# Optimization experiments

Measured on AMD Instinct MI355X. Metric: run time of the kernel, lower is better.

The kernel has to match this reference:

```python
import jax, jax.numpy as jnp
import numpy as np

N_HEAD = 16
WINDOW = 16  # fixed_window_size


def setup_inputs() -> dict:
    key = jax.random.key(0)
    k1, k2, k3 = jax.random.split(key, 3)
    B, T, C = 2, 2048, 1024
    x = jax.random.normal(k1, (B, T, C), dtype=jnp.float32)
    # torch Linear(C, 3C, bias=False): y = x @ W.T with W [3C, C].
    # We store the pre-transposed [C, 3C] matrix so y = x @ w_qkv.
    w_qkv = jax.random.normal(k2, (C, 3 * C), dtype=jnp.float32) * (1.0 / np.sqrt(C))
    w_proj = jax.random.normal(k3, (C, C), dtype=jnp.float32) * (1.0 / np.sqrt(C))
    return {"x": x, "w_qkv": w_qkv, "w_proj": w_proj}


def reference(x, w_qkv, w_proj):
    B, T, C = x.shape
    H, D = N_HEAD, C // N_HEAD
    qkv = x @ w_qkv  # [B, T, 3C]
    q, k, v = jnp.split(qkv, 3, axis=-1)
    # [B, T, C] -> [B, H, T, D]
    q, k, v = (t.reshape(B, T, H, D).transpose(0, 2, 1, 3) for t in (q, k, v))
    att = jnp.einsum("bhtd,bhsd->bhts", q, k) * (1.0 / np.sqrt(D))  # [B,H,T,T]
    # Mask exactly as the torch module builds it: tril ones, then zero where
    # col - row >= fixed_window_size (note: col-row, per the source).
    row = jnp.arange(T)[:, None]
    col = jnp.arange(T)[None, :]
    mask = (col <= row) & ~(col - row >= WINDOW)  # [T, T] bool
    att = jnp.where(mask[None, None, :, :], att, -jnp.inf)
    att = jax.nn.softmax(att, axis=-1)
    y = jnp.einsum("bhts,bhsd->bhtd", att, v)  # [B,H,T,D]
    y = y.transpose(0, 2, 1, 3).reshape(B, T, C)
    return y @ w_proj
```

## Files before the change

### kernel.cpp

```cpp
#include <hip/hip_runtime.h>
#include <stdint.h>

#define LOG2E 1.4426950408889634f
#define QSCALE 0.18033688011112042f

typedef __attribute__((ext_vector_type(8))) short bf16x8;
typedef __attribute__((ext_vector_type(4))) float f32x4;
typedef __attribute__((ext_vector_type(8))) unsigned short u16x8;

#define B_ 2
#define T_ 2048
#define C_ 1024
#define H_ 16
#define D_ 64
#define BT_ 4096
#define N3_ 3072

#if __has_builtin(__builtin_amdgcn_exp2f)
#define EXP2(x) __builtin_amdgcn_exp2f(x)
#else
#define EXP2(x) exp2f(x)
#endif

__device__ __forceinline__ unsigned short f2bf(float f) {
  union { float f; unsigned u; } x; x.f = f;
  return (unsigned short)((x.u + 0x7fffu + ((x.u >> 16) & 1u)) >> 16);
}
__device__ __forceinline__ float bf2f(unsigned short u) {
  union { unsigned u; float f; } x; x.u = ((unsigned)u) << 16;
  return x.f;
}
__device__ __forceinline__ unsigned f2u(float f) {
  union { float f; unsigned u; } x; x.f = f; return x.u;
}
__device__ __forceinline__ unsigned pack_bf2(float a, float b) {
  return __builtin_amdgcn_perm(f2u(b) + 0x8000u, f2u(a) + 0x8000u, 0x07060302u);
}

__device__ __forceinline__ void gld16(const unsigned short* g, unsigned short* l) {
  __builtin_amdgcn_global_load_lds(
      (const __attribute__((address_space(1))) unsigned int*)g,
      (__attribute__((address_space(3))) unsigned int*)l, 16, 0, 0);
}

__device__ __forceinline__ void tr32(const float* __restrict__ in,
                                     unsigned short* __restrict__ out,
                                     int K, int N, int b, int nbx, int tid) {
  __shared__ unsigned short tile[32][33];
  const int bx = b % nbx, by = b / nbx;
  const int n0 = bx * 32, k0 = by * 32;
  const int tx = tid & 31, ty = (tid >> 5) * 4;
#pragma unroll
  for (int r = 0; r < 4; r++)
    tile[ty + r][tx] = f2bf(in[(size_t)(k0 + ty + r) * N + n0 + tx]);
  __syncthreads();
#pragma unroll
  for (int r = 0; r < 4; r++)
    out[(size_t)(n0 + ty + r) * K + k0 + tx] = tile[tx][ty + r];
}

__global__ __launch_bounds__(256) void prep_kernel(
    const float* __restrict__ x, unsigned short* __restrict__ xb,
    const float* __restrict__ wq, unsigned short* __restrict__ wqT,
    const float* __restrict__ wp, unsigned short* __restrict__ wpT) {
  const int bid = blockIdx.x, tid = threadIdx.x;
  if (bid < 4096) {
    int i = (bid * 256 + tid) * 4;
    float4 v = *(const float4*)(x + i);
    ushort4 o;
    o.x = f2bf(v.x); o.y = f2bf(v.y); o.z = f2bf(v.z); o.w = f2bf(v.w);
    *(ushort4*)(xb + i) = o;
  } else if (bid < 4096 + 3072) {
    tr32(wq, wqT, 1024, 3072, bid - 4096, 96, tid);
  } else {
    tr32(wp, wpT, 1024, 1024, bid - 7168, 32, tid);
  }
}

template <int MODE>
__global__ __launch_bounds__(256) void gemm_kernel(
    const unsigned short* __restrict__ A, const unsigned short* __restrict__ Bt,
    unsigned short* __restrict__ qo, unsigned short* __restrict__ ko,
    unsigned short* __restrict__ vo, float* __restrict__ fo) {
  __shared__ unsigned short As[128 * 64];
  const int tid = threadIdx.x;
  const int wave = tid >> 6, lane = tid & 63;
  const int quad = lane >> 4, l16 = lane & 15;
  const int wm = (wave >> 1) * 64, wn = (wave & 1) * 32;
  const int m0 = blockIdx.y * 128, n0 = blockIdx.x * 64;

  f32x4 acc[4][2] = {};

  const unsigned short* Bp0 = Bt + (size_t)(n0 + wn + l16) * 1024 + quad * 8;
  const unsigned short* Bp1 = Bp0 + 16 * 1024;

  for (int k = 0; k < 1024; k += 64) {
    __syncthreads();
#pragma unroll
    for (int i = 0; i < 4; i++) {
      const int s = tid + 256 * i;
      const int row = s >> 3, ch = s & 7;
      gld16(A + (size_t)(m0 + row) * 1024 + k + ((ch ^ (row & 7)) * 8), As + s * 8);
    }
    bf16x8 b00 = *(const bf16x8*)(Bp0 + k);
    bf16x8 b01 = *(const bf16x8*)(Bp1 + k);
    bf16x8 b10 = *(const bf16x8*)(Bp0 + k + 32);
    bf16x8 b11 = *(const bf16x8*)(Bp1 + k + 32);
    __syncthreads();
#pragma unroll
    for (int sub = 0; sub < 2; sub++) {
      bf16x8 af[4];
#pragma unroll
      for (int mi = 0; mi < 4; mi++) {
        const int row = wm + mi * 16 + l16;
        af[mi] = *(const bf16x8*)(As + row * 64 + (((sub * 4 + quad) ^ (row & 7)) * 8));
      }
      const bf16x8 bz0 = sub ? b10 : b00;
      const bf16x8 bz1 = sub ? b11 : b01;
#pragma unroll
      for (int mi = 0; mi < 4; mi++) {
        acc[mi][0] = __builtin_amdgcn_mfma_f32_16x16x32_bf16(af[mi], bz0, acc[mi][0], 0, 0, 0);
        acc[mi][1] = __builtin_amdgcn_mfma_f32_16x16x32_bf16(af[mi], bz1, acc[mi][1], 0, 0, 0);
      }
    }
  }

  if (MODE == 0) {
    const int part = n0 >> 10;
    const int hh = (n0 >> 6) & 15;
#pragma unroll
    for (int mi = 0; mi < 4; mi++) {
#pragma unroll
      for (int r = 0; r < 4; r++) {
        const int m = m0 + wm + mi * 16 + quad * 4 + r;
        const int b = m >> 11, t = m & 2047;
#pragma unroll
        for (int ni = 0; ni < 2; ni++) {
          const int d = wn + ni * 16 + l16;
          float val = acc[mi][ni][r];
          if (part == 0) val *= QSCALE;
          const unsigned short bv = f2bf(val);
          if (part == 0)
            qo[((size_t)(b * H_ + hh) * T_ + t) * D_ + d] = bv;
          else if (part == 1)
            ko[((size_t)(b * H_ + hh) * T_ + t) * D_ + d] = bv;
          else
            vo[((size_t)(b * H_ + hh) * D_ + d) * T_ + t] = bv;
        }
      }
    }
  } else {
#pragma unroll
    for (int mi = 0; mi < 4; mi++)
#pragma unroll
      for (int r = 0; r < 4; r++) {
        const int m = m0 + wm + mi * 16 + quad * 4 + r;
#pragma unroll
        for (int ni = 0; ni < 2; ni++)
          fo[(size_t)m * 1024 + n0 + wn + ni * 16 + l16] = acc[mi][ni][r];
      }
  }
}

__global__ __launch_bounds__(256) void attn_kernel(
    const unsigned short* __restrict__ qb, const unsigned short* __restrict__ kb,
    const unsigned short* __restrict__ vb, unsigned short* __restrict__ yb,
    unsigned short* __restrict__ po, float* __restrict__ pl) {
  const int tid = threadIdx.x;
  const int wave = tid >> 6, lane = tid & 63;
  const int quad = lane >> 4, l16 = lane & 15;

  const int bid = blockIdx.x;
  const int bh = bid & 31;
  const int u = 62 - (bid >> 5);
  int qs, c, nch;
  if (u < 11) { qs = u; c = 0; nch = 1; }
  else if (u < 33) { int v = u - 11; qs = 11 + (v >> 1); c = v & 1; nch = 2; }
  else { int v = u - 33; qs = 22 + v / 3; c = v % 3; nch = 3; }
  const int nt = qs + 1;
  const int j0 = c * nt / nch, j1 = (c + 1) * nt / nch;
  const int b = bh >> 4, h = bh & 15;

  __shared__ unsigned short Ks[64 * 64];
  __shared__ unsigned short Vt[64 * 64];
  __shared__ unsigned short Ps[4 * 16 * 68];
  unsigned short* Pw = Ps + wave * 16 * 68;

  const unsigned short* Qg = qb + (size_t)bh * T_ * D_;
  const unsigned short* Kg = kb + (size_t)bh * T_ * D_;
  const unsigned short* Vg = vb + (size_t)bh * D_ * T_;

  const unsigned short* qp = Qg + (size_t)(qs * 64 + wave * 16 + l16) * D_ + quad * 8;
  bf16x8 qf0 = *(const bf16x8*)qp, qf1 = *(const bf16x8*)(qp + 32);

  f32x4 o[4] = {};
  float lacc = 0.f;
  const int qglob = qs * 64 + wave * 16 + l16;
  const int sloc_base = quad * 4;

  const int trow = tid >> 3, tch = tid & 7;

  for (int jt = j0; jt < j1; jt++) {
    const int s0 = jt * 64;
    __syncthreads();
    {
      const int r0 = trow, r1 = trow + 32;
      gld16(Kg + (size_t)(s0 + r0) * D_ + ((tch ^ (r0 & 7)) * 8), Ks + r0 * 64 + tch * 8);
      gld16(Kg + (size_t)(s0 + r1) * D_ + ((tch ^ (r1 & 7)) * 8), Ks + r1 * 64 + tch * 8);
      gld16(Vg + (size_t)r0 * T_ + s0 + ((tch ^ (r0 & 7)) * 8), Vt + r0 * 64 + tch * 8);
      gld16(Vg + (size_t)r1 * T_ + s0 + ((tch ^ (r1 & 7)) * 8), Vt + r1 * 64 + tch * 8);
    }
    __syncthreads();

    f32x4 s[4];
#pragma unroll
    for (int mi = 0; mi < 4; mi++) {
      const int row = mi * 16 + l16, sw = row & 7;
      bf16x8 kf0 = *(const bf16x8*)(Ks + row * 64 + ((quad ^ sw) * 8));
      bf16x8 kf1 = *(const bf16x8*)(Ks + row * 64 + (((quad + 4) ^ sw) * 8));
      f32x4 z = {0.f, 0.f, 0.f, 0.f};
      z = __builtin_amdgcn_mfma_f32_16x16x32_bf16(kf0, qf0, z, 0, 0, 0);
      s[mi] = __builtin_amdgcn_mfma_f32_16x16x32_bf16(kf1, qf1, z, 0, 0, 0);
    }

    if (jt == qs) {
#pragma unroll
      for (int mi = 0; mi < 4; mi++)
#pragma unroll
        for (int r = 0; r < 4; r++) {
          float p = EXP2(s[mi][r]);
          p = (s0 + mi * 16 + sloc_base + r > qglob) ? 0.f : p;
          s[mi][r] = p;
          lacc += p;
        }
    } else {
#pragma unroll
      for (int mi = 0; mi < 4; mi++)
#pragma unroll
        for (int r = 0; r < 4; r++) {
          float p = EXP2(s[mi][r]);
          s[mi][r] = p;
          lacc += p;
        }
    }

#pragma unroll
    for (int mi = 0; mi < 4; mi++) {
      unsigned d0 = pack_bf2(s[mi][0], s[mi][1]);
      unsigned d1 = pack_bf2(s[mi][2], s[mi][3]);
      *(uint2*)(Pw + l16 * 68 + mi * 16 + quad * 4) = make_uint2(d0, d1);
    }

#pragma unroll
    for (int kk = 0; kk < 2; kk++) {
      bf16x8 pf = *(const bf16x8*)(Pw + l16 * 68 + kk * 32 + quad * 8);
#pragma unroll
      for (int ni = 0; ni < 4; ni++) {
        const int row = ni * 16 + l16, sw = row & 7;
        bf16x8 vf = *(const bf16x8*)(Vt + row * 64 + (((kk * 4 + quad) ^ sw) * 8));
        o[ni] = __builtin_amdgcn_mfma_f32_16x16x32_bf16(pf, vf, o[ni], 0, 0, 0);
      }
    }
  }

  lacc += __shfl_xor(lacc, 16, 64);
  lacc += __shfl_xor(lacc, 32, 64);
  float lr[4];
#pragma unroll
  for (int r = 0; r < 4; r++) lr[r] = __shfl(lacc, quad * 4 + r, 16);

  if (nch == 1) {
#pragma unroll
    for (int r = 0; r < 4; r++) {
      float inv = 1.0f / lr[r];
      int tq = qs * 64 + wave * 16 + quad * 4 + r;
#pragma unroll
      for (int ni = 0; ni < 4; ni++)
        yb[((size_t)(b * T_ + tq)) * 1024 + h * 64 + ni * 16 + l16] = f2bf(o[ni][r] * inv);
    }
  } else {
    const int slot = 52 * bh + ((qs <= 21) ? ((qs - 11) * 2 + c) : (22 + (qs - 22) * 3 + c));
    unsigned short* pob = po + (size_t)slot * 4096;
#pragma unroll
    for (int r = 0; r < 4; r++) {
      const int row64 = wave * 16 + quad * 4 + r;
#pragma unroll
      for (int ni = 0; ni < 4; ni++)
        pob[row64 * 64 + ni * 16 + l16] = f2bf(o[ni][r]);
      if (l16 == 0) pl[slot * 64 + row64] = lr[r];
    }
  }
}

__global__ __launch_bounds__(256) void reduce_kernel(
    const unsigned short* __restrict__ po, const float* __restrict__ pl,
    unsigned short* __restrict__ yb) {
  int idx = blockIdx.x * 256 + threadIdx.x;
  int bh = idx / 21504;
  int rem = idx - bh * 21504;
  int rr = rem >> 4, cg = rem & 15;
  int qs = 11 + (rr >> 6), row64 = rr & 63;
  int base, nch;
  if (qs <= 21) { base = (qs - 11) * 2; nch = 2; }
  else { base = 22 + (qs - 22) * 3; nch = 3; }
  int b = bh >> 4, h = bh & 15;
  float a0 = 0.f, a1 = 0.f, a2 = 0.f, a3 = 0.f, l = 0.f;
  for (int cc = 0; cc < nch; cc++) {
    int slot = 52 * bh + base + cc;
    const unsigned short* p = po + (size_t)slot * 4096 + row64 * 64 + cg * 4;
    ushort4 uv = *(const ushort4*)p;
    a0 += bf2f(uv.x); a1 += bf2f(uv.y); a2 += bf2f(uv.z); a3 += bf2f(uv.w);
    l += pl[slot * 64 + row64];
  }
  float inv = 1.0f / l;
  int tq = qs * 64 + row64;
  ushort4 w;
  w.x = f2bf(a0 * inv); w.y = f2bf(a1 * inv); w.z = f2bf(a2 * inv); w.w = f2bf(a3 * inv);
  *(ushort4*)(yb + ((size_t)(b * T_ + tq)) * 1024 + h * 64 + cg * 4) = w;
}

extern "C" void kernel_launch(void* const* d_in, const int* in_sizes, int n_in,
                              void* d_out, int out_size, void* d_ws, size_t ws_size,
                              hipStream_t stream) {
  const float* x = (const float*)d_in[0];
  const float* w_qkv = (const float*)d_in[1];
  const float* w_proj = (const float*)d_in[2];
  float* out = (float*)d_out;

  unsigned short* xb = (unsigned short*)d_ws;
  unsigned short* wprojT = xb + (size_t)BT_ * C_;
  unsigned short* qb = wprojT + (size_t)C_ * C_;
  unsigned short* kb = qb + (size_t)B_ * H_ * T_ * D_;
  unsigned short* vb = kb + (size_t)B_ * H_ * T_ * D_;
  unsigned short* wqkvT = vb + (size_t)B_ * H_ * T_ * D_;
  unsigned short* po = wqkvT;
  float* pl = (float*)(po + (size_t)1664 * 4096);
  unsigned short* yb = xb;

  prep_kernel<<<dim3(8192), 256, 0, stream>>>(x, xb, w_qkv, wqkvT, w_proj, wprojT);

  gemm_kernel<0><<<dim3(N3_ / 64, BT_ / 128), 256, 0, stream>>>(xb, wqkvT, qb, kb, vb, nullptr);
  attn_kernel<<<dim3(32 * 63), 256, 0, stream>>>(qb, kb, vb, yb, po, pl);
  reduce_kernel<<<dim3(2688), 256, 0, stream>>>(po, pl, yb);
  gemm_kernel<1><<<dim3(C_ / 64, BT_ / 128), 256, 0, stream>>>(yb, wprojT, nullptr, nullptr, nullptr, out);
}
```

Measured before the change: 218.9 us.

## Stage B tiles in LDS and split-K the output projection GEMM

The shared GEMM kernel now stages the B (weight) tile through swizzled LDS with async global-to-LDS loads instead of per-lane direct global loads. A new gemm2 kernel for the output projection uses 512 threads, two wave groups each handling half of K, and combines the partial accumulators through LDS before writing. This targets the low occupancy of the projection GEMM, which has only 512 blocks, and the uncoalesced B loads, at the cost of more LDS use and an extra reduction step.

```diff
diff --git a/kernel.cpp b/kernel.cpp
--- a/kernel.cpp
+++ b/kernel.cpp
@@ -83,6 +83,7 @@
     unsigned short* __restrict__ qo, unsigned short* __restrict__ ko,
     unsigned short* __restrict__ vo, float* __restrict__ fo) {
   __shared__ unsigned short As[128 * 64];
+  __shared__ unsigned short Bs[64 * 64];
   const int tid = threadIdx.x;
   const int wave = tid >> 6, lane = tid & 63;
   const int quad = lane >> 4, l16 = lane & 15;
@@ -91,9 +92,6 @@
 
   f32x4 acc[4][2] = {};
 
-  const unsigned short* Bp0 = Bt + (size_t)(n0 + wn + l16) * 1024 + quad * 8;
-  const unsigned short* Bp1 = Bp0 + 16 * 1024;
-
   for (int k = 0; k < 1024; k += 64) {
     __syncthreads();
 #pragma unroll
@@ -102,26 +100,31 @@
       const int row = s >> 3, ch = s & 7;
       gld16(A + (size_t)(m0 + row) * 1024 + k + ((ch ^ (row & 7)) * 8), As + s * 8);
     }
-    bf16x8 b00 = *(const bf16x8*)(Bp0 + k);
-    bf16x8 b01 = *(const bf16x8*)(Bp1 + k);
-    bf16x8 b10 = *(const bf16x8*)(Bp0 + k + 32);
-    bf16x8 b11 = *(const bf16x8*)(Bp1 + k + 32);
+#pragma unroll
+    for (int i = 0; i < 2; i++) {
+      const int s = tid + 256 * i;
+      const int row = s >> 3, ch = s & 7;
+      gld16(Bt + (size_t)(n0 + row) * 1024 + k + ((ch ^ (row & 7)) * 8), Bs + s * 8);
+    }
     __syncthreads();
 #pragma unroll
     for (int sub = 0; sub < 2; sub++) {
-      bf16x8 af[4];
+      bf16x8 af[4], bfr[2];
 #pragma unroll
       for (int mi = 0; mi < 4; mi++) {
         const int row = wm + mi * 16 + l16;
         af[mi] = *(const bf16x8*)(As + row * 64 + (((sub * 4 + quad) ^ (row & 7)) * 8));
       }
-      const bf16x8 bz0 = sub ? b10 : b00;
-      const bf16x8 bz1 = sub ? b11 : b01;
-#pragma unroll
-      for (int mi = 0; mi < 4; mi++) {
-        acc[mi][0] = __builtin_amdgcn_mfma_f32_16x16x32_bf16(af[mi], bz0, acc[mi][0], 0, 0, 0);
-        acc[mi][1] = __builtin_amdgcn_mfma_f32_16x16x32_bf16(af[mi], bz1, acc[mi][1], 0, 0, 0);
-      }
+#pragma unroll
+      for (int ni = 0; ni < 2; ni++) {
+        const int row = wn + ni * 16 + l16;
+        bfr[ni] = *(const bf16x8*)(Bs + row * 64 + (((sub * 4 + quad) ^ (row & 7)) * 8));
+      }
+#pragma unroll
+      for (int mi = 0; mi < 4; mi++)
+#pragma unroll
+        for (int ni = 0; ni < 2; ni++)
+          acc[mi][ni] = __builtin_amdgcn_mfma_f32_16x16x32_bf16(af[mi], bfr[ni], acc[mi][ni], 0, 0, 0);
     }
   }
 
@@ -159,6 +162,88 @@
         for (int ni = 0; ni < 2; ni++)
           fo[(size_t)m * 1024 + n0 + wn + ni * 16 + l16] = acc[mi][ni][r];
       }
+  }
+}
+
+__global__ __launch_bounds__(512) void gemm2_kernel(
+    const unsigned short* __restrict__ A, const unsigned short* __restrict__ Bt,
+    float* __restrict__ fo) {
+  __shared__ unsigned short As[2][128 * 64];
+  __shared__ unsigned short Bs[2][64 * 64];
+  const int tid = threadIdx.x;
+  const int wave = tid >> 6, lane = tid & 63;
+  const int quad = lane >> 4, l16 = lane & 15;
+  const int grp = wave >> 2, w4 = wave & 3;
+  const int wm = (w4 >> 1) * 64, wn = (w4 & 1) * 32;
+  const int m0 = blockIdx.y * 128, n0 = blockIdx.x * 64;
+  const int gtid = tid & 255;
+
+  f32x4 acc[4][2] = {};
+  const int kbase = grp * 512;
+  unsigned short* Asg = &As[grp][0];
+  unsigned short* Bsg = &Bs[grp][0];
+
+  for (int kk = 0; kk < 512; kk += 64) {
+    const int k = kbase + kk;
+    __syncthreads();
+#pragma unroll
+    for (int i = 0; i < 4; i++) {
+      const int s = gtid + 256 * i;
+      const int row = s >> 3, ch = s & 7;
+      gld16(A + (size_t)(m0 + row) * 1024 + k + ((ch ^ (row & 7)) * 8), Asg + s * 8);
+    }
+#pragma unroll
+    for (int i = 0; i < 2; i++) {
+      const int s = gtid + 256 * i;
+      const int row = s >> 3, ch = s & 7;
+      gld16(Bt + (size_t)(n0 + row) * 1024 + k + ((ch ^ (row & 7)) * 8), Bsg + s * 8);
+    }
+    __syncthreads();
+#pragma unroll
+    for (int sub = 0; sub < 2; sub++) {
+      bf16x8 af[4], bfr[2];
+#pragma unroll
+      for (int mi = 0; mi < 4; mi++) {
+        const int row = wm + mi * 16 + l16;
+        af[mi] = *(const bf16x8*)(Asg + row * 64 + (((sub * 4 + quad) ^ (row & 7)) * 8));
+      }
+#pragma unroll
+      for (int ni = 0; ni < 2; ni++) {
+        const int row = wn + ni * 16 + l16;
+        bfr[ni] = *(const bf16x8*)(Bsg + row * 64 + (((sub * 4 + quad) ^ (row & 7)) * 8));
+      }
+#pragma unroll
+      for (int mi = 0; mi < 4; mi++)
+#pragma unroll
+        for (int ni = 0; ni < 2; ni++)
+          acc[mi][ni] = __builtin_amdgcn_mfma_f32_16x16x32_bf16(af[mi], bfr[ni], acc[mi][ni], 0, 0, 0);
+    }
+  }
+
+  __syncthreads();
+  float* comb = (float*)&As[0][0];
+  if (grp == 1) {
+#pragma unroll
+    for (int mi = 0; mi < 4; mi++)
+#pragma unroll
+      for (int ni = 0; ni < 2; ni++)
+        *(f32x4*)(comb + ((w4 * 8 + mi * 2 + ni) * 256 + lane * 4)) = acc[mi][ni];
+  }
+  __syncthreads();
+  if (grp == 0) {
+#pragma unroll
+    for (int mi = 0; mi < 4; mi++) {
+#pragma unroll
+      for (int ni = 0; ni < 2; ni++) {
+        f32x4 oth = *(const f32x4*)(comb + ((w4 * 8 + mi * 2 + ni) * 256 + lane * 4));
+        f32x4 v = acc[mi][ni] + oth;
+#pragma unroll
+        for (int r = 0; r < 4; r++) {
+          const int m = m0 + wm + mi * 16 + quad * 4 + r;
+          fo[(size_t)m * 1024 + n0 + wn + ni * 16 + l16] = v[r];
+        }
+      }
+    }
   }
 }
 
@@ -342,5 +427,5 @@
   gemm_kernel<0><<<dim3(N3_ / 64, BT_ / 128), 256, 0, stream>>>(xb, wqkvT, qb, kb, vb, nullptr);
   attn_kernel<<<dim3(32 * 63), 256, 0, stream>>>(qb, kb, vb, yb, po, pl);
   reduce_kernel<<<dim3(2688), 256, 0, stream>>>(po, pl, yb);
-  gemm_kernel<1><<<dim3(C_ / 64, BT_ / 128), 256, 0, stream>>>(yb, wprojT, nullptr, nullptr, nullptr, out);
-}
+  gemm2_kernel<<<dim3(C_ / 64, BT_ / 128), 512, 0, stream>>>(yb, wprojT, out);
+}
```

After: 183.6 us. 16.1% less time.
